# Performance work log

Measured on AMD Instinct MI355X. Metric: run time of the kernel, lower is better.

The kernel has to match this reference:

```python
import jax, jax.numpy as jnp
import numpy as np

N_NODES = 50000
N_EDGES = 1600000
FEAT = 64


def setup_inputs() -> dict:
    key = jax.random.key(0)
    k1, k2, k3, k4 = jax.random.split(key, 4)
    nodes = jax.random.normal(k1, (N_NODES, FEAT), dtype=jnp.float32)
    neighbor_feats = jax.random.normal(k2, (N_EDGES, FEAT), dtype=jnp.float32)
    attention = jax.random.uniform(k3, (N_EDGES,), dtype=jnp.float32)
    bias = jnp.zeros((FEAT,), dtype=jnp.float32)  # init_params zero-inits bias
    segment_ids = jnp.sort(jax.random.randint(k4, (N_EDGES,), 0, N_NODES, dtype=jnp.int32))
    return {"nodes": nodes, "neighbor_feats": neighbor_feats, "attention": attention,
            "bias": bias, "segment_ids": segment_ids}


def reference(nodes, neighbor_feats, attention, bias, segment_ids):
    # Per node i: sum_j attn[i,j] * neigh[i,j]  (ragged loop in torch ->
    # fused weighted segment-sum over the flattened edge list), then + bias.
    weighted = neighbor_feats * attention[:, None]          # [E, F]
    out = jax.ops.segment_sum(weighted, segment_ids, num_segments=N_NODES)  # [N, F]
    return out + bias
```

## Files before the change

kernel.cpp:

```cpp
#include <hip/hip_runtime.h>


#define N_NODES 50000
#define N_EDGES 1600000
#define FEAT 64

__global__ __launch_bounds__(256) void segsum_kernel(
    const float* __restrict__ neigh,
    const float* __restrict__ att,
    const float* __restrict__ bias,
    const int*   __restrict__ seg,
    float* __restrict__ out,
    int n_edges, int n_nodes)
{
    const int wave_id = (blockIdx.x * blockDim.x + threadIdx.x) >> 6;
    const int lane    = threadIdx.x & 63;
    if (wave_id >= n_nodes) return;
    const int node = wave_id;

    {
    }
    const int target = node + (lane & 1);
    int lo = 0, hi = n_edges;
    while (lo < hi) {
        const int mid = (lo + hi) >> 1;
        if (seg[mid] < target) lo = mid + 1; else hi = mid;
    }
    const int start = __shfl(lo, 0);
    const int end   = __shfl(lo, 1);

    const int rowgrp = lane >> 4;
    const int colgrp = lane & 15;

    float4 acc = make_float4(0.f, 0.f, 0.f, 0.f);

    int e = start;
    for (; e + 4 <= end; e += 4) {
        const int r = e + rowgrp;
        const float a = att[r];
        const float4 v = *(const float4*)(neigh + (size_t)r * FEAT + colgrp * 4);
        acc.x = fmaf(a, v.x, acc.x);
        acc.y = fmaf(a, v.y, acc.y);
        acc.z = fmaf(a, v.z, acc.z);
        acc.w = fmaf(a, v.w, acc.w);
    }
    if (e + rowgrp < end) {
        const int r = e + rowgrp;
        const float a = att[r];
        const float4 v = *(const float4*)(neigh + (size_t)r * FEAT + colgrp * 4);
        acc.x = fmaf(a, v.x, acc.x);
        acc.y = fmaf(a, v.y, acc.y);
        acc.z = fmaf(a, v.z, acc.z);
        acc.w = fmaf(a, v.w, acc.w);
    }

    #pragma unroll
    for (int off = 32; off >= 16; off >>= 1) {
        acc.x += __shfl_down(acc.x, off);
        acc.y += __shfl_down(acc.y, off);
        acc.z += __shfl_down(acc.z, off);
        acc.w += __shfl_down(acc.w, off);
    }

    if (rowgrp == 0) {
        const float4 b = *(const float4*)(bias + colgrp * 4);
        float4 o;
        o.x = acc.x + b.x;
        o.y = acc.y + b.y;
        o.z = acc.z + b.z;
        o.w = acc.w + b.w;
        *(float4*)(out + (size_t)node * FEAT + colgrp * 4) = o;
    }
}

extern "C" void kernel_launch(void* const* d_in, const int* in_sizes, int n_in,
                              void* d_out, int out_size, void* d_ws, size_t ws_size,
                              hipStream_t stream) {
    const float* neigh = (const float*)d_in[1];
    const float* att   = (const float*)d_in[2];
    const float* bias  = (const float*)d_in[3];
    const int*   seg   = (const int*)d_in[4];
    float* out = (float*)d_out;

    const int n_edges = in_sizes[2];
    const int n_nodes = out_size / FEAT;

    const int waves_per_block = 256 / 64;
    const int blocks = (n_nodes + waves_per_block - 1) / waves_per_block;
    segsum_kernel<<<blocks, 256, 0, stream>>>(neigh, att, bias, seg, out,
                                              n_edges, n_nodes);
}
```

Baseline: 582.9 us.

## Precompute CSR offsets in a separate kernel and unroll edge loop by two

Adds a boundaries kernel that turns the sorted segment ids into a CSR offset array in workspace, replacing the per-wave binary search over 1.6M ids. The main loop now processes 8 edges per iteration with two accumulators to raise memory-level parallelism. The cost is an extra kernel launch, an extra pass over the segment ids, and a dependence on workspace size.

Measured after the change: 546.7 us. -6.2%, faster.

```diff
diff --git a/kernel.cpp b/kernel.cpp
--- a/kernel.cpp
+++ b/kernel.cpp
@@ -1,58 +1,92 @@
 #include <hip/hip_runtime.h>
 
 
-#define N_NODES 50000
-#define N_EDGES 1600000
 #define FEAT 64
+
+__global__ __launch_bounds__(256) void boundaries_kernel(
+    const int* __restrict__ seg,
+    int* __restrict__ offs,
+    int n_edges, int n_nodes)
+{
+    const int e = blockIdx.x * blockDim.x + threadIdx.x;
+    if (e >= n_edges) return;
+    const int s = seg[e];
+    if (e == 0) {
+        for (int n = 0; n <= s; ++n) offs[n] = 0;
+    } else {
+        const int sp = seg[e - 1];
+        if (sp != s)
+            for (int n = sp + 1; n <= s; ++n) offs[n] = e;
+    }
+    if (e == n_edges - 1) {
+        for (int n = s + 1; n <= n_nodes; ++n) offs[n] = n_edges;
+    }
+}
 
 __global__ __launch_bounds__(256) void segsum_kernel(
     const float* __restrict__ neigh,
     const float* __restrict__ att,
     const float* __restrict__ bias,
-    const int*   __restrict__ seg,
+    const int*   __restrict__ offs,
     float* __restrict__ out,
-    int n_edges, int n_nodes)
+    int n_nodes)
 {
     const int wave_id = (blockIdx.x * blockDim.x + threadIdx.x) >> 6;
     const int lane    = threadIdx.x & 63;
     if (wave_id >= n_nodes) return;
     const int node = wave_id;
 
-    {
-    }
-    const int target = node + (lane & 1);
-    int lo = 0, hi = n_edges;
-    while (lo < hi) {
-        const int mid = (lo + hi) >> 1;
-        if (seg[mid] < target) lo = mid + 1; else hi = mid;
-    }
-    const int start = __shfl(lo, 0);
-    const int end   = __shfl(lo, 1);
+    const int start = offs[node];
+    const int end   = offs[node + 1];
 
     const int rowgrp = lane >> 4;
     const int colgrp = lane & 15;
 
-    float4 acc = make_float4(0.f, 0.f, 0.f, 0.f);
+    float4 acc0 = make_float4(0.f, 0.f, 0.f, 0.f);
+    float4 acc1 = make_float4(0.f, 0.f, 0.f, 0.f);
 
     int e = start;
-    for (; e + 4 <= end; e += 4) {
+    for (; e + 8 <= end; e += 8) {
+        const int r0 = e + rowgrp;
+        const int r1 = e + 4 + rowgrp;
+        const float  a0 = att[r0];
+        const float4 v0 = *(const float4*)(neigh + (size_t)r0 * FEAT + colgrp * 4);
+        const float  a1 = att[r1];
+        const float4 v1 = *(const float4*)(neigh + (size_t)r1 * FEAT + colgrp * 4);
+        acc0.x = fmaf(a0, v0.x, acc0.x);
+        acc0.y = fmaf(a0, v0.y, acc0.y);
+        acc0.z = fmaf(a0, v0.z, acc0.z);
+        acc0.w = fmaf(a0, v0.w, acc0.w);
+        acc1.x = fmaf(a1, v1.x, acc1.x);
+        acc1.y = fmaf(a1, v1.y, acc1.y);
+        acc1.z = fmaf(a1, v1.z, acc1.z);
+        acc1.w = fmaf(a1, v1.w, acc1.w);
+    }
+    if (e + 4 <= end) {
         const int r = e + rowgrp;
-        const float a = att[r];
+        const float  a = att[r];
         const float4 v = *(const float4*)(neigh + (size_t)r * FEAT + colgrp * 4);
-        acc.x = fmaf(a, v.x, acc.x);
-        acc.y = fmaf(a, v.y, acc.y);
-        acc.z = fmaf(a, v.z, acc.z);
-        acc.w = fmaf(a, v.w, acc.w);
+        acc0.x = fmaf(a, v.x, acc0.x);
+        acc0.y = fmaf(a, v.y, acc0.y);
+        acc0.z = fmaf(a, v.z, acc0.z);
+        acc0.w = fmaf(a, v.w, acc0.w);
+        e += 4;
     }
     if (e + rowgrp < end) {
         const int r = e + rowgrp;
-        const float a = att[r];
+        const float  a = att[r];
         const float4 v = *(const float4*)(neigh + (size_t)r * FEAT + colgrp * 4);
-        acc.x = fmaf(a, v.x, acc.x);
-        acc.y = fmaf(a, v.y, acc.y);
-        acc.z = fmaf(a, v.z, acc.z);
-        acc.w = fmaf(a, v.w, acc.w);
+        acc1.x = fmaf(a, v.x, acc1.x);
+        acc1.y = fmaf(a, v.y, acc1.y);
+        acc1.z = fmaf(a, v.z, acc1.z);
+        acc1.w = fmaf(a, v.w, acc1.w);
     }
+
+    float4 acc;
+    acc.x = acc0.x + acc1.x;
+    acc.y = acc0.y + acc1.y;
+    acc.z = acc0.z + acc1.z;
+    acc.w = acc0.w + acc1.w;
 
     #pragma unroll
     for (int off = 32; off >= 16; off >>= 1) {
@@ -85,8 +119,13 @@
     const int n_edges = in_sizes[2];
     const int n_nodes = out_size / FEAT;
 
+    int* offs = (int*)d_ws;
+
+    boundaries_kernel<<<(n_edges + 255) / 256, 256, 0, stream>>>(
+        seg, offs, n_edges, n_nodes);
+
     const int waves_per_block = 256 / 64;
     const int blocks = (n_nodes + waves_per_block - 1) / waves_per_block;
-    segsum_kernel<<<blocks, 256, 0, stream>>>(neigh, att, bias, seg, out,
-                                              n_edges, n_nodes);
+    segsum_kernel<<<blocks, 256, 0, stream>>>(neigh, att, bias, offs, out,
+                                              n_nodes);
 }
```
